# Kernel tuning notes

Hardware: AMD Instinct MI355X
Metric: run time of the kernel (lower is better)

The kernel has to match this reference:

```python
import jax, jax.numpy as jnp
import numpy as np

COMMITMENT_COST = 0.25
NUM_EMBEDDINGS = 8192
EMBEDDING_DIM = 256
N_TOKENS = 32768


def setup_inputs() -> dict:
    key = jax.random.key(0)
    k1, k2 = jax.random.split(key)
    inputs = jax.random.normal(k1, (N_TOKENS, EMBEDDING_DIM), dtype=jnp.float32)
    embed = jax.random.normal(k2, (EMBEDDING_DIM, NUM_EMBEDDINGS), dtype=jnp.float32)
    return {"inputs": inputs, "embed": embed}


def reference(inputs, embed):
    # inputs: [N, D], embed: [D, K]
    input_shape = inputs.shape
    flat = inputs.reshape(-1, embed.shape[0])
    input_norm = jnp.sum(flat * flat, axis=1, keepdims=True)
    embed_norm = jnp.sum(embed * embed, axis=0, keepdims=True)
    distances = input_norm + embed_norm - 2.0 * (flat @ embed)
    encoding_indices = jnp.argmin(distances, axis=1)  # [N]
    # direct gather instead of one-hot matmul (same math)
    quantized = jnp.take(embed.T, encoding_indices, axis=0).reshape(input_shape)
    e_latent_loss = jnp.mean((jax.lax.stop_gradient(quantized) - inputs) ** 2)
    loss = COMMITMENT_COST * e_latent_loss
    # straight-through estimator
    quantized_st = inputs + jax.lax.stop_gradient(quantized - inputs)
    return quantized_st, loss, encoding_indices
```

## Files before the change

### kernel.cpp

```cpp
#include <hip/hip_runtime.h>

#define N_TOK 32768
#define DIM   256
#define NEMB  8192

#define MARGIN_A  0.2f
#define MARGIN_T2 0.008f
#define MARGIN_B  0.0625f
#define GROUP 8
#define KSPLIT 4

typedef _Float16 f16;
typedef __attribute__((ext_vector_type(4))) _Float16 f16x4;
typedef __attribute__((ext_vector_type(8))) _Float16 f16x8;
typedef __attribute__((ext_vector_type(4))) float     f32x4;

__global__ void enorm_kernel(const float* __restrict__ E, float* __restrict__ enorm) {
    int k = blockIdx.x * blockDim.x + threadIdx.x;
    float s = 0.f;
#pragma unroll 8
    for (int d = 0; d < DIM; ++d) {
        float e = E[d * NEMB + k];
        s = fmaf(e, e, s);
    }
    enorm[k] = s;
}

__global__ __launch_bounds__(256) void cvt3_kernel(const float* __restrict__ E,
                                                   f16* __restrict__ ET,
                                                   f16* __restrict__ ETlo,
                                                   float* __restrict__ ET32,
                                                   int wlo, int wf32) {
    __shared__ float shf[64][65];
    const int tid = threadIdx.x;
    const int k0 = (blockIdx.x & 127) * 64;
    const int d0 = (blockIdx.x >> 7) * 64;
#pragma unroll
    for (int i = 0; i < 16; ++i) {
        int flat = i * 256 + tid;
        int k = flat & 63, d = flat >> 6;
        shf[k][d] = E[(size_t)(d0 + d) * NEMB + k0 + k];
    }
    __syncthreads();
#pragma unroll
    for (int i = 0; i < 16; ++i) {
        int flat = i * 256 + tid;
        int d = flat & 63, kk = flat >> 6;
        float v = shf[kk][d];
        f16 hi = (f16)v;
        ET[(size_t)(k0 + kk) * DIM + d0 + d] = hi;
        if (wlo)  ETlo[(size_t)(k0 + kk) * DIM + d0 + d] = (f16)(v - (float)hi);
        if (wf32) ET32[(size_t)(k0 + kk) * DIM + d0 + d] = v;
    }
}

__device__ __forceinline__ void gload_lds16(const void* g, void* l) {
    __builtin_amdgcn_global_load_lds(
        (const __attribute__((address_space(1))) unsigned int*)g,
        (__attribute__((address_space(3))) unsigned int*)l, 16, 0, 0);
}

__global__ __launch_bounds__(512, 2) void argmin_f16v5_kernel(
        const float* __restrict__ X, const f16* __restrict__ ET,
        const float* __restrict__ enorm,
        int* __restrict__ idx1o, int* __restrict__ idx2o, int* __restrict__ flago) {
    __shared__ char smem[131072];

    const int tid = threadIdx.x;
    const int w   = tid >> 6;
    const int l   = tid & 63;
    const int l15 = l & 15, l4 = l >> 4;
    const int h   = w & 1;
    const int cs  = w >> 1;
    const int r0  = blockIdx.x * 128;

    {
        const float4* X4 = (const float4*)(X + (size_t)r0 * DIM);
        f16* xs = (f16*)smem;
#pragma unroll
        for (int i = 0; i < 16; ++i) {
            int flat4 = tid + i * 512;
            float4 v = X4[flat4];
            int row = flat4 >> 6, d4 = flat4 & 63;
            f16x4 p = {(f16)v.x, (f16)v.y, (f16)v.z, (f16)v.w};
            *(f16x4*)(xs + row * 256 + d4 * 4) = p;
        }
    }
    __syncthreads();

    f16x8 Afr[4][8];
    {
        const f16* xs = (const f16*)smem;
#pragma unroll
        for (int mt = 0; mt < 4; ++mt)
#pragma unroll
            for (int c = 0; c < 8; ++c)
                Afr[mt][c] = *(const f16x8*)(xs + (h * 64 + mt * 16 + l15) * 256 + c * 32 + l4 * 8);
    }
    __syncthreads();

    float m1v[4][4], m2v[4][4];
    int   i1v[4][4];
#pragma unroll
    for (int mt = 0; mt < 4; ++mt)
#pragma unroll
        for (int rg = 0; rg < 4; ++rg) {
            m1v[mt][rg] = 3.4e38f; m2v[mt][rg] = 3.4e38f; i1v[mt][rg] = 0x7fffffff;
        }

    auto stagePair = [&](int pt, int buf) {
#pragma unroll
        for (int t = 0; t < 2; ++t) {
            const int kt = pt * 2 + t;
#pragma unroll
            for (int j = 0; j < 4; ++j) {
                const int code = w * 8 + j * 2 + (l >> 5);
                const f16* src = ET + ((size_t)kt * 64 + code) * 256
                                   + (((l & 31) ^ (code & 7)) << 3);
                char* dst = smem + buf * 65536 + t * 32768 + (w * 8 + j * 2) * 512;
                gload_lds16(src, dst);
            }
        }
    };

    const int codeL = cs * 16 + l15;
    stagePair(0, 0);
    int p = 0;
    for (int pt = 0; pt < 64; ++pt) {
        __syncthreads();
        if (pt + 1 < 64) stagePair(pt + 1, p ^ 1);

#pragma unroll
        for (int t = 0; t < 2; ++t) {
            const int kt = pt * 2 + t;
            f32x4 acc[4];
#pragma unroll
            for (int mt = 0; mt < 4; ++mt) acc[mt] = (f32x4){0.f, 0.f, 0.f, 0.f};

            const f16* bb = (const f16*)(smem + p * 65536 + t * 32768);
#pragma unroll
            for (int c = 0; c < 8; ++c) {
                const int g = (c * 4 + l4) ^ (l15 & 7);
                f16x8 b = *(const f16x8*)(bb + codeL * 256 + g * 8);
#pragma unroll
                for (int mt = 0; mt < 4; ++mt)
                    acc[mt] = __builtin_amdgcn_mfma_f32_16x16x32_f16(Afr[mt][c], b, acc[mt], 0, 0, 0);
            }

            const int code = kt * 64 + codeL;
            const float en = enorm[code];
#pragma unroll
            for (int mt = 0; mt < 4; ++mt)
#pragma unroll
                for (int rg = 0; rg < 4; ++rg) {
                    float v = fmaf(-2.f, acc[mt][rg], en);
                    bool cl = v < m1v[mt][rg];
                    m2v[mt][rg] = fminf(m2v[mt][rg], fmaxf(m1v[mt][rg], v));
                    i1v[mt][rg] = cl ? code : i1v[mt][rg];
                    m1v[mt][rg] = fminf(m1v[mt][rg], v);
                }
        }
        p ^= 1;
    }

#pragma unroll
    for (int off = 1; off < 16; off <<= 1) {
#pragma unroll
        for (int mt = 0; mt < 4; ++mt)
#pragma unroll
            for (int rg = 0; rg < 4; ++rg) {
                float om1 = __shfl_xor(m1v[mt][rg], off);
                int   oi1 = __shfl_xor(i1v[mt][rg], off);
                float om2 = __shfl_xor(m2v[mt][rg], off);
                bool sw = (om1 < m1v[mt][rg]) ||
                          (om1 == m1v[mt][rg] && oi1 < i1v[mt][rg]);
                float hi = sw ? m1v[mt][rg] : om1;
                m1v[mt][rg] = sw ? om1 : m1v[mt][rg];
                i1v[mt][rg] = sw ? oi1 : i1v[mt][rg];
                m2v[mt][rg] = fminf(fminf(m2v[mt][rg], om2), hi);
            }
    }

    __syncthreads();
    float* sm1 = (float*)smem;
    int*   si1 = (int*)(smem + 2048);
    float* sm2 = (float*)(smem + 4096);
    if (l15 == 0) {
#pragma unroll
        for (int mt = 0; mt < 4; ++mt)
#pragma unroll
            for (int rg = 0; rg < 4; ++rg) {
                int row = h * 64 + mt * 16 + l4 * 4 + rg;
                sm1[row * 4 + cs] = m1v[mt][rg];
                si1[row * 4 + cs] = i1v[mt][rg];
                sm2[row * 4 + cs] = m2v[mt][rg];
            }
    }
    __syncthreads();
    if (tid < 128) {
        float M1 = 3.4e38f, M2 = 3.4e38f;
        int   I1 = 0x7fffffff;
#pragma unroll
        for (int e = 0; e < 4; ++e) {
            float v = sm1[tid * 4 + e]; int vi = si1[tid * 4 + e];
            if (v < M1 || (v == M1 && vi < I1)) { M2 = M1; M1 = v; I1 = vi; }
            else M2 = fminf(M2, v);
            M2 = fminf(M2, sm2[tid * 4 + e]);
        }
        int r = r0 + tid;
        idx1o[r] = I1;
        idx2o[r] = I1;
        flago[r] = (M2 - M1 < MARGIN_A) ? -1 : 0;
    }
}

__global__ __launch_bounds__(256) void compact_kernel(const int* __restrict__ flago,
        int* __restrict__ list, int* __restrict__ countp) {
    __shared__ int cnts[256], bases[256];
    const int tid = threadIdx.x;
    int c = 0;
    for (int i = 0; i < N_TOK / 256; ++i)
        c += (flago[tid * (N_TOK / 256) + i] < 0) ? 1 : 0;
    cnts[tid] = c;
    __syncthreads();
    if (tid == 0) {
        int run = 0;
        for (int t = 0; t < 256; ++t) { bases[t] = run; run += cnts[t]; }
        countp[0] = run;
    }
    __syncthreads();
    int o = bases[tid];
    for (int i = 0; i < N_TOK / 256; ++i) {
        int r = tid * (N_TOK / 256) + i;
        if (flago[r] < 0) list[o++] = r;
    }
}

__global__ __launch_bounds__(512) void rescan_split_kernel(
        const float* __restrict__ X, const f16* __restrict__ ET,
        const f16* __restrict__ ETlo, const float* __restrict__ enorm,
        const int* __restrict__ list, const int* __restrict__ countp,
        float* __restrict__ pm1, float* __restrict__ pm2, float* __restrict__ pm3,
        int* __restrict__ pi1, int* __restrict__ pi2) {
    __shared__ char smem[131072];
    const int cnt = countp[0];
    const int rb  = blockIdx.x >> 3;
    const int ks  = blockIdx.x & 7;
    if (rb * 64 >= cnt) return;

    const int tid = threadIdx.x, w = tid >> 6, l = tid & 63;
    const int l15 = l & 15, l4 = l >> 4;
    const int h = w & 1, cs = w >> 1;

    f16x8 Ah[2][8], Al[2][8];
#pragma unroll
    for (int mt = 0; mt < 2; ++mt) {
        int jg  = rb * 64 + h * 32 + mt * 16 + l15;
        int row = list[jg < cnt ? jg : cnt - 1];
        const float* xp = X + (size_t)row * DIM + l4 * 8;
#pragma unroll
        for (int c = 0; c < 8; ++c) {
            float4 v0 = *(const float4*)(xp + c * 32);
            float4 v1 = *(const float4*)(xp + c * 32 + 4);
            float xv[8] = {v0.x, v0.y, v0.z, v0.w, v1.x, v1.y, v1.z, v1.w};
            f16x8 hi, lo;
#pragma unroll
            for (int i = 0; i < 8; ++i) {
                f16 hv = (f16)xv[i];
                hi[i] = hv;
                lo[i] = (f16)(xv[i] - (float)hv);
            }
            Ah[mt][c] = hi; Al[mt][c] = lo;
        }
    }

    float m1v[2][4], m2v[2][4], m3v[2][4];
    int   i1v[2][4], i2v[2][4];
#pragma unroll
    for (int mt = 0; mt < 2; ++mt)
#pragma unroll
        for (int rg = 0; rg < 4; ++rg) {
            m1v[mt][rg] = 3.4e38f; m2v[mt][rg] = 3.4e38f; m3v[mt][rg] = 3.4e38f;
            i1v[mt][rg] = 0x7fffffff; i2v[mt][rg] = 0x7fffffff;
        }

    auto stage = [&](int kt, int buf) {
        const int tile = ks * 16 + kt;
#pragma unroll
        for (int j = 0; j < 4; ++j) {
            const int code = w * 8 + j * 2 + (l >> 5);
            size_t off = ((size_t)tile * 64 + code) * 256 + (((l & 31) ^ (code & 7)) << 3);
            char* dsth = smem + buf * 65536 + (w * 8 + j * 2) * 512;
            gload_lds16(ET + off, dsth);
            gload_lds16(ETlo + off, dsth + 32768);
        }
    };

    const int codeL = cs * 16 + l15;
    stage(0, 0);
    int p = 0;
    for (int kt = 0; kt < 16; ++kt) {
        __syncthreads();
        if (kt + 1 < 16) stage(kt + 1, p ^ 1);

        f32x4 acc[2];
#pragma unroll
        for (int mt = 0; mt < 2; ++mt) acc[mt] = (f32x4){0.f, 0.f, 0.f, 0.f};

        const f16* bh = (const f16*)(smem + p * 65536);
        const f16* bl = (const f16*)(smem + p * 65536 + 32768);
#pragma unroll
        for (int c = 0; c < 8; ++c) {
            const int g = (c * 4 + l4) ^ (l15 & 7);
            f16x8 vh = *(const f16x8*)(bh + codeL * 256 + g * 8);
            f16x8 vl = *(const f16x8*)(bl + codeL * 256 + g * 8);
#pragma unroll
            for (int mt = 0; mt < 2; ++mt) {
                acc[mt] = __builtin_amdgcn_mfma_f32_16x16x32_f16(Ah[mt][c], vh, acc[mt], 0, 0, 0);
                acc[mt] = __builtin_amdgcn_mfma_f32_16x16x32_f16(Ah[mt][c], vl, acc[mt], 0, 0, 0);
                acc[mt] = __builtin_amdgcn_mfma_f32_16x16x32_f16(Al[mt][c], vh, acc[mt], 0, 0, 0);
            }
        }

        const int code = (ks * 16 + kt) * 64 + codeL;
        const float en = enorm[code];
#pragma unroll
        for (int mt = 0; mt < 2; ++mt)
#pragma unroll
            for (int rg = 0; rg < 4; ++rg) {
                float v = fmaf(-2.f, acc[mt][rg], en);
                if (v < m1v[mt][rg]) {
                    m3v[mt][rg] = m2v[mt][rg];
                    m2v[mt][rg] = m1v[mt][rg]; i2v[mt][rg] = i1v[mt][rg];
                    m1v[mt][rg] = v;           i1v[mt][rg] = code;
                } else if (v < m2v[mt][rg]) {
                    m3v[mt][rg] = m2v[mt][rg];
                    m2v[mt][rg] = v;           i2v[mt][rg] = code;
                } else if (v < m3v[mt][rg]) {
                    m3v[mt][rg] = v;
                }
            }
        p ^= 1;
    }

    __syncthreads();
    float* Mm1 = (float*)smem;
    int*   Mi1 = (int*)(smem + 16384);
    float* Mm2 = (float*)(smem + 32768);
    int*   Mi2 = (int*)(smem + 49152);
    float* Mm3 = (float*)(smem + 65536);
#pragma unroll
    for (int mt = 0; mt < 2; ++mt)
#pragma unroll
        for (int rg = 0; rg < 4; ++rg) {
            int row = h * 32 + mt * 16 + l4 * 4 + rg;
            int e   = cs * 16 + l15;
            Mm1[row * 64 + e] = m1v[mt][rg];
            Mi1[row * 64 + e] = i1v[mt][rg];
            Mm2[row * 64 + e] = m2v[mt][rg];
            Mi2[row * 64 + e] = i2v[mt][rg];
            Mm3[row * 64 + e] = m3v[mt][rg];
        }
    __syncthreads();
    if (tid < 64) {
        float a1 = 3.4e38f, a2 = 3.4e38f, a3 = 3.4e38f;
        int   ai1 = 0x7fffffff, ai2 = 0x7fffffff;
        for (int e = 0; e < 64; ++e) {
            float b1 = Mm1[tid * 64 + e], b2 = Mm2[tid * 64 + e], b3 = Mm3[tid * 64 + e];
            int   bi1 = Mi1[tid * 64 + e], bi2 = Mi2[tid * 64 + e];
            if (b1 < a1 || (b1 == a1 && bi1 < ai1)) { a3 = a2; a2 = a1; ai2 = ai1; a1 = b1; ai1 = bi1; }
            else if (b1 < a2 || (b1 == a2 && bi1 < ai2)) { a3 = a2; a2 = b1; ai2 = bi1; }
            else if (b1 < a3) a3 = b1;
            if (b2 < a1 || (b2 == a1 && bi2 < ai1)) { a3 = a2; a2 = a1; ai2 = ai1; a1 = b2; ai1 = bi2; }
            else if (b2 < a2 || (b2 == a2 && bi2 < ai2)) { a3 = a2; a2 = b2; ai2 = bi2; }
            else if (b2 < a3) a3 = b2;
            if (b3 < a3) a3 = b3;
        }
        int jg = rb * 64 + tid;
        if (jg < cnt) {
            pm1[jg * 8 + ks] = a1; pm2[jg * 8 + ks] = a2; pm3[jg * 8 + ks] = a3;
            pi1[jg * 8 + ks] = ai1; pi2[jg * 8 + ks] = ai2;
        }
    }
}

__global__ void merge3_kernel(const int* __restrict__ list, const int* __restrict__ countp,
        const float* __restrict__ pm1, const float* __restrict__ pm2,
        const float* __restrict__ pm3,
        const int* __restrict__ pi1, const int* __restrict__ pi2,
        int* __restrict__ idx1o, int* __restrict__ idx2o, int* __restrict__ flago) {
    const int gid = blockIdx.x * 256 + threadIdx.x;
    if (gid >= countp[0]) return;
    float a1 = 3.4e38f, a2 = 3.4e38f, a3 = 3.4e38f;
    int   ai1 = 0x7fffffff, ai2 = 0x7fffffff;
#pragma unroll
    for (int ks = 0; ks < 8; ++ks) {
        float b1 = pm1[gid * 8 + ks], b2 = pm2[gid * 8 + ks], b3 = pm3[gid * 8 + ks];
        int   bi1 = pi1[gid * 8 + ks], bi2 = pi2[gid * 8 + ks];
        if (b1 < a1 || (b1 == a1 && bi1 < ai1)) { a3 = a2; a2 = a1; ai2 = ai1; a1 = b1; ai1 = bi1; }
        else if (b1 < a2 || (b1 == a2 && bi1 < ai2)) { a3 = a2; a2 = b1; ai2 = bi1; }
        else if (b1 < a3) a3 = b1;
        if (b2 < a1 || (b2 == a1 && bi2 < ai1)) { a3 = a2; a2 = a1; ai2 = ai1; a1 = b2; ai1 = bi2; }
        else if (b2 < a2 || (b2 == a2 && bi2 < ai2)) { a3 = a2; a2 = b2; ai2 = bi2; }
        else if (b2 < a3) a3 = b2;
        if (b3 < a3) a3 = b3;
    }
    const int row = list[gid];
    int fl = 0;
    if (a2 - a1 < MARGIN_T2) fl = (a3 - a1 < MARGIN_T2) ? 2 : 1;
    idx1o[row] = ai1; idx2o[row] = ai2; flago[row] = fl;
}

__global__ __launch_bounds__(256) void rescan_group_kernel(
        const float* __restrict__ X, const float* __restrict__ E,
        const float* __restrict__ enorm,
        const int* __restrict__ list, const int* __restrict__ countp,
        float* __restrict__ pm1, float* __restrict__ pm2, float* __restrict__ pm3,
        int* __restrict__ pi1, int* __restrict__ pi2) {
    const int cnt = countp[0];
    const int rc  = blockIdx.x >> 2;
    const int ks  = blockIdx.x & 3;
    if (rc * GROUP >= cnt) return;
    const int tid = threadIdx.x;
    __shared__ int rows_s[GROUP];
    __shared__ float sm1[256], sm2[256], sm3[256];
    __shared__ int   si1[256], si2[256];
    if (tid < GROUP) {
        int j = rc * GROUP + tid;
        rows_s[tid] = list[j < cnt ? j : cnt - 1];
    }
    __syncthreads();
    int rowsg[GROUP];
#pragma unroll
    for (int rr = 0; rr < GROUP; ++rr)
        rowsg[rr] = __builtin_amdgcn_readfirstlane(rows_s[rr]);

    float m1[GROUP], m2[GROUP], m3[GROUP];
    int   i1[GROUP], i2[GROUP];
#pragma unroll
    for (int rr = 0; rr < GROUP; ++rr) {
        m1[rr] = 3.4e38f; m2[rr] = 3.4e38f; m3[rr] = 3.4e38f;
        i1[rr] = 0x7fffffff; i2[rr] = 0x7fffffff;
    }
    for (int j = 0; j < 8; ++j) {
        const int k = ks * 2048 + j * 256 + tid;
        float acc[GROUP];
#pragma unroll
        for (int rr = 0; rr < GROUP; ++rr) acc[rr] = 0.f;
#pragma unroll 1
        for (int dc = 0; dc < 8; ++dc) {
            float ev[32];
#pragma unroll
            for (int i = 0; i < 32; ++i) ev[i] = E[(size_t)(dc * 32 + i) * NEMB + k];
#pragma unroll
            for (int rr = 0; rr < GROUP; ++rr) {
                const float* xp = X + (size_t)rowsg[rr] * DIM + dc * 32;
#pragma unroll
                for (int i = 0; i < 32; ++i) acc[rr] = fmaf(ev[i], xp[i], acc[rr]);
            }
        }
        const float en = enorm[k];
#pragma unroll
        for (int rr = 0; rr < GROUP; ++rr) {
            float v = fmaf(-2.f, acc[rr], en);
            if (v < m1[rr])      { m3[rr] = m2[rr]; m2[rr] = m1[rr]; i2[rr] = i1[rr]; m1[rr] = v; i1[rr] = k; }
            else if (v < m2[rr]) { m3[rr] = m2[rr]; m2[rr] = v; i2[rr] = k; }
            else if (v < m3[rr]) { m3[rr] = v; }
        }
    }
#pragma unroll 1
    for (int rr = 0; rr < GROUP; ++rr) {
        sm1[tid] = m1[rr]; sm2[tid] = m2[rr]; sm3[tid] = m3[rr];
        si1[tid] = i1[rr]; si2[tid] = i2[rr];
        __syncthreads();
        for (int st = 128; st > 0; st >>= 1) {
            if (tid < st) {
                float a1 = sm1[tid], a2 = sm2[tid], a3 = sm3[tid];
                int   ai1 = si1[tid], ai2 = si2[tid];
                float b1 = sm1[tid + st], b2 = sm2[tid + st], b3 = sm3[tid + st];
                int   bi1 = si1[tid + st], bi2 = si2[tid + st];
                if (b1 < a1 || (b1 == a1 && bi1 < ai1)) { a3 = a2; a2 = a1; ai2 = ai1; a1 = b1; ai1 = bi1; }
                else if (b1 < a2 || (b1 == a2 && bi1 < ai2)) { a3 = a2; a2 = b1; ai2 = bi1; }
                else if (b1 < a3) a3 = b1;
                if (b2 < a1 || (b2 == a1 && bi2 < ai1)) { a3 = a2; a2 = a1; ai2 = ai1; a1 = b2; ai1 = bi2; }
                else if (b2 < a2 || (b2 == a2 && bi2 < ai2)) { a3 = a2; a2 = b2; ai2 = bi2; }
                else if (b2 < a3) a3 = b2;
                if (b3 < a3) a3 = b3;
                sm1[tid] = a1; sm2[tid] = a2; sm3[tid] = a3; si1[tid] = ai1; si2[tid] = ai2;
            }
            __syncthreads();
        }
        if (tid == 0) {
            int jg = rc * GROUP + rr;
            if (jg < cnt) {
                pm1[jg * KSPLIT + ks] = sm1[0]; pm2[jg * KSPLIT + ks] = sm2[0];
                pm3[jg * KSPLIT + ks] = sm3[0];
                pi1[jg * KSPLIT + ks] = si1[0]; pi2[jg * KSPLIT + ks] = si2[0];
            }
        }
        __syncthreads();
    }
}

__global__ void merge_kernel(const int* __restrict__ list, const int* __restrict__ countp,
        const float* __restrict__ pm1, const float* __restrict__ pm2,
        const float* __restrict__ pm3,
        const int* __restrict__ pi1, const int* __restrict__ pi2,
        int* __restrict__ idx1o, int* __restrict__ idx2o, int* __restrict__ flago) {
    const int gid = blockIdx.x * 256 + threadIdx.x;
    if (gid >= countp[0]) return;
    float a1 = 3.4e38f, a2 = 3.4e38f, a3 = 3.4e38f;
    int   ai1 = 0x7fffffff, ai2 = 0x7fffffff;
#pragma unroll
    for (int ks = 0; ks < KSPLIT; ++ks) {
        float b1 = pm1[gid * KSPLIT + ks], b2 = pm2[gid * KSPLIT + ks], b3 = pm3[gid * KSPLIT + ks];
        int   bi1 = pi1[gid * KSPLIT + ks], bi2 = pi2[gid * KSPLIT + ks];
        if (b1 < a1 || (b1 == a1 && bi1 < ai1)) { a3 = a2; a2 = a1; ai2 = ai1; a1 = b1; ai1 = bi1; }
        else if (b1 < a2 || (b1 == a2 && bi1 < ai2)) { a3 = a2; a2 = b1; ai2 = bi1; }
        else if (b1 < a3) a3 = b1;
        if (b2 < a1 || (b2 == a1 && bi2 < ai1)) { a3 = a2; a2 = a1; ai2 = ai1; a1 = b2; ai1 = bi2; }
        else if (b2 < a2 || (b2 == a2 && bi2 < ai2)) { a3 = a2; a2 = b2; ai2 = bi2; }
        else if (b2 < a3) a3 = b2;
        if (b3 < a3) a3 = b3;
    }
    const int row = list[gid];
    int fl = 0;
    if (a2 - a1 < MARGIN_B) fl = (a3 - a1 < MARGIN_B) ? 2 : 1;
    idx1o[row] = ai1; idx2o[row] = ai2; flago[row] = fl;
}

#define BM 64
#define BN 128
#define DC 32
#define TM 4
#define TN 8
__global__ __launch_bounds__(256, 2) void argmin_f32_kernel(
        const float* __restrict__ X, const float* __restrict__ E,
        const float* __restrict__ enorm,
        int* __restrict__ idx1o, int* __restrict__ idx2o, int* __restrict__ flago) {
    __shared__ float As[DIM * BM];
    __shared__ float Bs[DC * BN];
    const int tid = threadIdx.x;
    const int r0  = blockIdx.x * BM;
    {
        const float4* X4 = (const float4*)(X + (size_t)r0 * DIM);
#pragma unroll
        for (int i = 0; i < 16; ++i) {
            int flat = tid + i * 256;
            int row = flat >> 6, c4 = flat & 63;
            float4 v = X4[flat];
            int d = c4 * 4;
            As[(d + 0) * BM + row] = v.x;
            As[(d + 1) * BM + row] = v.y;
            As[(d + 2) * BM + row] = v.z;
            As[(d + 3) * BM + row] = v.w;
        }
    }
    const int tc = tid & 15;
    const int tr = tid >> 4;
    float m1[TM], m2[TM], m3[TM];
    int   i1[TM], i2[TM];
#pragma unroll
    for (int j = 0; j < TM; ++j) { m1[j] = m2[j] = m3[j] = 3.4e38f; i1[j] = i2[j] = 0x7fffffff; }
    for (int kt = 0; kt < NEMB; kt += BN) {
        float acc[TM][TN];
#pragma unroll
        for (int j = 0; j < TM; ++j)
#pragma unroll
            for (int i = 0; i < TN; ++i) acc[j][i] = 0.f;
        for (int dc = 0; dc < DIM; dc += DC) {
            __syncthreads();
            const float4* E4 = (const float4*)E;
#pragma unroll
            for (int i = 0; i < 4; ++i) {
                int flat = tid + i * 256;
                int dd = flat >> 5, k4 = flat & 31;
                float4 v = E4[(size_t)(dc + dd) * (NEMB / 4) + (kt >> 2) + k4];
                *(float4*)&Bs[dd * BN + k4 * 4] = v;
            }
            __syncthreads();
#pragma unroll
            for (int dd = 0; dd < DC; ++dd) {
                float4 av = *(const float4*)&As[(dc + dd) * BM + tr * TM];
                float4 b0 = *(const float4*)&Bs[dd * BN + tc * TN];
                float4 b1 = *(const float4*)&Bs[dd * BN + tc * TN + 4];
                float a[TM] = {av.x, av.y, av.z, av.w};
                float b[TN] = {b0.x, b0.y, b0.z, b0.w, b1.x, b1.y, b1.z, b1.w};
#pragma unroll
                for (int j = 0; j < TM; ++j)
#pragma unroll
                    for (int i = 0; i < TN; ++i)
                        acc[j][i] = fmaf(a[j], b[i], acc[j][i]);
            }
        }
        float4 e0 = *(const float4*)&enorm[kt + tc * TN];
        float4 e1 = *(const float4*)&enorm[kt + tc * TN + 4];
        float en[TN] = {e0.x, e0.y, e0.z, e0.w, e1.x, e1.y, e1.z, e1.w};
#pragma unroll
        for (int j = 0; j < TM; ++j) {
#pragma unroll
            for (int i = 0; i < TN; ++i) {
                float v = en[i] - 2.f * acc[j][i];
                int k = kt + tc * TN + i;
                if (v < m1[j]) { m3[j] = m2[j]; m2[j] = m1[j]; i2[j] = i1[j]; m1[j] = v; i1[j] = k; }
                else if (v < m2[j]) { m3[j] = m2[j]; m2[j] = v; i2[j] = k; }
                else if (v < m3[j]) { m3[j] = v; }
            }
        }
    }
    __syncthreads();
    float* Mm1 = As;
    float* Mm2 = As + 1024;
    float* Mm3 = As + 2048;
    int*   Mi1 = (int*)(As + 3072);
    int*   Mi2 = (int*)(As + 4096);
#pragma unroll
    for (int j = 0; j < TM; ++j) {
        int row = tr * TM + j;
        Mm1[row * 16 + tc] = m1[j];
        Mm2[row * 16 + tc] = m2[j];
        Mm3[row * 16 + tc] = m3[j];
        Mi1[row * 16 + tc] = i1[j];
        Mi2[row * 16 + tc] = i2[j];
    }
    __syncthreads();
    if (tid < BM) {
        float M1 = 3.4e38f, M2 = 3.4e38f, M3 = 3.4e38f;
        int I1 = 0x7fffffff, I2 = 0x7fffffff;
        for (int e = 0; e < 16; ++e) {
            float v = Mm1[tid * 16 + e]; int vi = Mi1[tid * 16 + e];
            if (v < M1 || (v == M1 && vi < I1)) { M3 = M2; M2 = M1; I2 = I1; M1 = v; I1 = vi; }
            else if (v < M2 || (v == M2 && vi < I2)) { M3 = M2; M2 = v; I2 = vi; }
            else if (v < M3) { M3 = v; }
            v = Mm2[tid * 16 + e]; vi = Mi2[tid * 16 + e];
            if (v < M1 || (v == M1 && vi < I1)) { M3 = M2; M2 = M1; I2 = I1; M1 = v; I1 = vi; }
            else if (v < M2 || (v == M2 && vi < I2)) { M3 = M2; M2 = v; I2 = vi; }
            else if (v < M3) { M3 = v; }
            v = Mm3[tid * 16 + e];
            if (v < M3) M3 = v;
        }
        int r = r0 + tid;
        int fl = 0;
        if (M2 - M1 < MARGIN_B) fl = (M3 - M1 < MARGIN_B) ? 2 : 1;
        idx1o[r] = I1; idx2o[r] = I2; flago[r] = fl;
    }
}

__global__ __launch_bounds__(256) void refine_kernel(
        const float* __restrict__ X, const float* __restrict__ E,
        int* __restrict__ idx1o, const int* __restrict__ idx2o,
        const int* __restrict__ flago) {
    __shared__ double redA[256];
    __shared__ double redB[256];
    __shared__ int    redI[256];
    const int tid = threadIdx.x;
    for (int rr = 0; rr < 8; ++rr) {
        int r = blockIdx.x * 8 + rr;
        int flag = flago[r];
        if (flag == 0) continue;
        if (flag == 1) {
            int a = idx1o[r], b = idx2o[r];
            double x  = (double)X[(size_t)r * DIM + tid];
            double ea = (double)E[(size_t)tid * NEMB + a];
            double eb = (double)E[(size_t)tid * NEMB + b];
            redA[tid] = ea * (ea - 2.0 * x);
            redB[tid] = eb * (eb - 2.0 * x);
            __syncthreads();
            for (int s = 128; s > 0; s >>= 1) {
                if (tid < s) { redA[tid] += redA[tid + s]; redB[tid] += redB[tid + s]; }
                __syncthreads();
            }
            if (tid == 0) {
                double sa = redA[0], sb = redB[0];
                idx1o[r] = (sb < sa || (sb == sa && b < a)) ? b : a;
            }
            __syncthreads();
        } else {
            double bm = 1e300; int bi = 0x7fffffff;
            for (int k = tid; k < NEMB; k += 256) {
                double s = 0.0;
                for (int d = 0; d < DIM; ++d) {
                    double e = (double)E[(size_t)d * NEMB + k];
                    double x = (double)X[(size_t)r * DIM + d];
                    s += e * (e - 2.0 * x);
                }
                if (s < bm) { bm = s; bi = k; }
            }
            redA[tid] = bm; redI[tid] = bi;
            __syncthreads();
            for (int s = 128; s > 0; s >>= 1) {
                if (tid < s) {
                    if (redA[tid + s] < redA[tid] ||
                        (redA[tid + s] == redA[tid] && redI[tid + s] < redI[tid])) {
                        redA[tid] = redA[tid + s]; redI[tid] = redI[tid + s];
                    }
                }
                __syncthreads();
            }
            if (tid == 0) idx1o[r] = redI[0];
            __syncthreads();
        }
    }
}

__global__ __launch_bounds__(256) void gather_kernel(
        const float* __restrict__ X, const float* __restrict__ E,
        const int* __restrict__ idx,
        float* __restrict__ outq, float* __restrict__ outidxf,
        double* __restrict__ partials) {
    __shared__ double red[256];
    const int tid = threadIdx.x;
    const int row = blockIdx.x * 4 + (tid >> 6);
    const int d0  = (tid & 63) * 4;
    const int k   = idx[row];
    float4 x = *(const float4*)&X[(size_t)row * DIM + d0];
    float q0 = E[(size_t)(d0 + 0) * NEMB + k];
    float q1 = E[(size_t)(d0 + 1) * NEMB + k];
    float q2 = E[(size_t)(d0 + 2) * NEMB + k];
    float q3 = E[(size_t)(d0 + 3) * NEMB + k];
    float4 q = {q0, q1, q2, q3};
    *(float4*)&outq[(size_t)row * DIM + d0] = q;
    if ((tid & 63) == 0) outidxf[row] = (float)k;
    double s = 0.0, t;
    t = (double)q0 - (double)x.x; s += t * t;
    t = (double)q1 - (double)x.y; s += t * t;
    t = (double)q2 - (double)x.z; s += t * t;
    t = (double)q3 - (double)x.w; s += t * t;
    red[tid] = s;
    __syncthreads();
    for (int st = 128; st > 0; st >>= 1) {
        if (tid < st) red[tid] += red[tid + st];
        __syncthreads();
    }
    if (tid == 0) partials[blockIdx.x] = red[0];
}

__global__ __launch_bounds__(256) void gather2_kernel(
        const float* __restrict__ X, const float* __restrict__ ET32,
        const int* __restrict__ idx,
        float* __restrict__ outq, float* __restrict__ outidxf,
        double* __restrict__ partials) {
    __shared__ double red[256];
    const int tid = threadIdx.x;
    const int row = blockIdx.x * 4 + (tid >> 6);
    const int d0  = (tid & 63) * 4;
    const int k   = idx[row];
    float4 x = *(const float4*)&X[(size_t)row * DIM + d0];
    float4 q = *(const float4*)&ET32[(size_t)k * DIM + d0];
    *(float4*)&outq[(size_t)row * DIM + d0] = q;
    if ((tid & 63) == 0) outidxf[row] = (float)k;
    double s = 0.0, t;
    t = (double)q.x - (double)x.x; s += t * t;
    t = (double)q.y - (double)x.y; s += t * t;
    t = (double)q.z - (double)x.z; s += t * t;
    t = (double)q.w - (double)x.w; s += t * t;
    red[tid] = s;
    __syncthreads();
    for (int st = 128; st > 0; st >>= 1) {
        if (tid < st) red[tid] += red[tid + st];
        __syncthreads();
    }
    if (tid == 0) partials[blockIdx.x] = red[0];
}

__global__ __launch_bounds__(256) void loss_kernel(const double* __restrict__ partials,
                                                   float* __restrict__ outloss) {
    __shared__ double red[256];
    const int tid = threadIdx.x;
    double s = 0.0;
    for (int i = tid; i < N_TOK / 4; i += 256) s += partials[i];
    red[tid] = s;
    __syncthreads();
    for (int st = 128; st > 0; st >>= 1) {
        if (tid < st) red[tid] += red[tid + st];
        __syncthreads();
    }
    if (tid == 0)
        outloss[0] = (float)(0.25 * red[0] / (double)((size_t)N_TOK * DIM));
}

extern "C" void kernel_launch(void* const* d_in, const int* in_sizes, int n_in,
                              void* d_out, int out_size, void* d_ws, size_t ws_size,
                              hipStream_t stream) {
    const float* X = (const float*)d_in[0];
    const float* E = (const float*)d_in[1];

    float* outq    = (float*)d_out;
    float* outloss = outq + (size_t)N_TOK * DIM;
    float* outidx  = outloss + 1;

    char* base = (char*)d_ws;
    float*  enorm    = (float*)base;
    int*    idx1     = (int*)(base + 32768);
    int*    idx2     = (int*)(base + 163840);
    int*    flag     = (int*)(base + 294912);
    double* partials = (double*)(base + 425984);
    f16*    ET       = (f16*)(base + 524288);
    char*   etbase   = base + 524288;
    int*    listB    = (int*)etbase;
    int*    countB   = (int*)(etbase + 131072);
    float*  pm1B     = (float*)(etbase + 132096);
    float*  pm2B     = (float*)(etbase + 132096 + 524288);
    float*  pm3B     = (float*)(etbase + 132096 + 1048576);
    int*    pi1B     = (int*)  (etbase + 132096 + 1572864);
    int*    pi2B     = (int*)  (etbase + 132096 + 2097152);
    f16*    ETlo     = (f16*)(base + 4718592);
    int*    listA    = (int*)(base + 8912896);
    int*    countA   = (int*)(base + 9043968);
    float*  ET32     = (float*)(base + 9044992);
    float*  pm1A     = outq;
    float*  pm2A     = outq + 262144;
    float*  pm3A     = outq + 524288;
    int*    pi1A     = (int*)(outq + 786432);
    int*    pi2A     = (int*)(outq + 1048576);
    const size_t NEED_B  = 4718592;
    const size_t NEED_A  = 12190720;
    const size_t NEED_A2 = 9044992 + (size_t)NEMB * DIM * sizeof(float);

    enorm_kernel<<<NEMB / 256, 256, 0, stream>>>(E, enorm);
    if (ws_size >= NEED_A) {
        const int wf32 = (ws_size >= NEED_A2) ? 1 : 0;
        cvt3_kernel        <<<512,        256, 0, stream>>>(E, ET, ETlo, ET32, 1, wf32);
        argmin_f16v5_kernel<<<N_TOK / 128, 512, 0, stream>>>(X, ET, enorm, idx1, idx2, flag);
        compact_kernel     <<<1,          256, 0, stream>>>(flag, listA, countA);
        rescan_split_kernel<<<512 * 8,    512, 0, stream>>>(X, ET, ETlo, enorm, listA, countA,
                                                            pm1A, pm2A, pm3A, pi1A, pi2A);
        merge3_kernel      <<<N_TOK / 256, 256, 0, stream>>>(listA, countA, pm1A, pm2A, pm3A,
                                                             pi1A, pi2A, idx1, idx2, flag);
        refine_kernel<<<N_TOK / 8, 256, 0, stream>>>(X, E, idx1, idx2, flag);
        if (wf32)
            gather2_kernel<<<N_TOK / 4, 256, 0, stream>>>(X, ET32, idx1, outq, outidx, partials);
        else
            gather_kernel <<<N_TOK / 4, 256, 0, stream>>>(X, E, idx1, outq, outidx, partials);
    } else if (ws_size >= NEED_B) {
        cvt3_kernel        <<<512,        256, 0, stream>>>(E, ET, ET, (float*)ET, 0, 0);
        argmin_f16v5_kernel<<<N_TOK / 128, 512, 0, stream>>>(X, ET, enorm, idx1, idx2, flag);
        compact_kernel     <<<1,          256, 0, stream>>>(flag, listB, countB);
        rescan_group_kernel<<<(N_TOK / GROUP) * KSPLIT, 256, 0, stream>>>(X, E, enorm, listB, countB,
                                                                          pm1B, pm2B, pm3B, pi1B, pi2B);
        merge_kernel       <<<N_TOK / 256, 256, 0, stream>>>(listB, countB, pm1B, pm2B, pm3B,
                                                             pi1B, pi2B, idx1, idx2, flag);
        refine_kernel<<<N_TOK / 8, 256, 0, stream>>>(X, E, idx1, idx2, flag);
        gather_kernel<<<N_TOK / 4, 256, 0, stream>>>(X, E, idx1, outq, outidx, partials);
    } else {
        argmin_f32_kernel  <<<N_TOK / BM, 256, 0, stream>>>(X, E, enorm, idx1, idx2, flag);
        refine_kernel<<<N_TOK / 8, 256, 0, stream>>>(X, E, idx1, idx2, flag);
        gather_kernel<<<N_TOK / 4, 256, 0, stream>>>(X, E, idx1, outq, outidx, partials);
    }
    loss_kernel  <<<1,         256, 0, stream>>>(partials, outloss);
}
```

Before: 292.3 us.

## Split codebook across two wave halves in 1024-thread argmin blocks

The argmin kernel now launches 1024 threads per block. Each set of 8 waves scans its own half of the codebook (4096 codes) through its own double-buffered 32KB LDS stage, instead of 8 waves walking all codes in pairs of tiles. The final cross-wave reduction grows from 4 to 8 candidates per row. The goal is to double the waves resident per CU under the same 128KB LDS footprint, so more MFMA and load latency can be hidden. The cost is more register pressure from the A fragments duplicated in both halves, and heavier barriers across 16 waves.

```diff
diff --git a/kernel.cpp b/kernel.cpp
--- a/kernel.cpp
+++ b/kernel.cpp
@@ -60,26 +60,28 @@
         (__attribute__((address_space(3))) unsigned int*)l, 16, 0, 0);
 }
 
-__global__ __launch_bounds__(512, 2) void argmin_f16v5_kernel(
+__global__ __launch_bounds__(1024, 4) void argmin_f16v6_kernel(
         const float* __restrict__ X, const f16* __restrict__ ET,
         const float* __restrict__ enorm,
         int* __restrict__ idx1o, int* __restrict__ idx2o, int* __restrict__ flago) {
     __shared__ char smem[131072];
 
-    const int tid = threadIdx.x;
-    const int w   = tid >> 6;
-    const int l   = tid & 63;
-    const int l15 = l & 15, l4 = l >> 4;
-    const int h   = w & 1;
-    const int cs  = w >> 1;
-    const int r0  = blockIdx.x * 128;
+    const int tid  = threadIdx.x;
+    const int w    = tid >> 6;
+    const int l    = tid & 63;
+    const int l15  = l & 15, l4 = l >> 4;
+    const int half = w >> 3;
+    const int w8   = w & 7;
+    const int h    = w8 & 1;
+    const int cs   = w8 >> 1;
+    const int r0   = blockIdx.x * 128;
 
     {
         const float4* X4 = (const float4*)(X + (size_t)r0 * DIM);
         f16* xs = (f16*)smem;
 #pragma unroll
-        for (int i = 0; i < 16; ++i) {
-            int flat4 = tid + i * 512;
+        for (int i = 0; i < 8; ++i) {
+            int flat4 = tid + i * 1024;
             float4 v = X4[flat4];
             int row = flat4 >> 6, d4 = flat4 & 63;
             f16x4 p = {(f16)v.x, (f16)v.y, (f16)v.z, (f16)v.w};
@@ -108,58 +110,50 @@
             m1v[mt][rg] = 3.4e38f; m2v[mt][rg] = 3.4e38f; i1v[mt][rg] = 0x7fffffff;
         }
 
-    auto stagePair = [&](int pt, int buf) {
-#pragma unroll
-        for (int t = 0; t < 2; ++t) {
-            const int kt = pt * 2 + t;
-#pragma unroll
-            for (int j = 0; j < 4; ++j) {
-                const int code = w * 8 + j * 2 + (l >> 5);
-                const f16* src = ET + ((size_t)kt * 64 + code) * 256
-                                   + (((l & 31) ^ (code & 7)) << 3);
-                char* dst = smem + buf * 65536 + t * 32768 + (w * 8 + j * 2) * 512;
-                gload_lds16(src, dst);
-            }
+    auto stage = [&](int kt, int buf) {
+#pragma unroll
+        for (int j = 0; j < 4; ++j) {
+            const int code = w8 * 8 + j * 2 + (l >> 5);
+            const f16* src = ET + ((size_t)(half * 4096 + kt * 64 + code)) * 256
+                               + (((l & 31) ^ (code & 7)) << 3);
+            char* dst = smem + half * 65536 + buf * 32768 + (w8 * 8 + j * 2) * 512;
+            gload_lds16(src, dst);
         }
     };
 
     const int codeL = cs * 16 + l15;
-    stagePair(0, 0);
+    stage(0, 0);
     int p = 0;
-    for (int pt = 0; pt < 64; ++pt) {
+    for (int kt = 0; kt < 64; ++kt) {
         __syncthreads();
-        if (pt + 1 < 64) stagePair(pt + 1, p ^ 1);
-
-#pragma unroll
-        for (int t = 0; t < 2; ++t) {
-            const int kt = pt * 2 + t;
-            f32x4 acc[4];
-#pragma unroll
-            for (int mt = 0; mt < 4; ++mt) acc[mt] = (f32x4){0.f, 0.f, 0.f, 0.f};
-
-            const f16* bb = (const f16*)(smem + p * 65536 + t * 32768);
-#pragma unroll
-            for (int c = 0; c < 8; ++c) {
-                const int g = (c * 4 + l4) ^ (l15 & 7);
-                f16x8 b = *(const f16x8*)(bb + codeL * 256 + g * 8);
-#pragma unroll
-                for (int mt = 0; mt < 4; ++mt)
-                    acc[mt] = __builtin_amdgcn_mfma_f32_16x16x32_f16(Afr[mt][c], b, acc[mt], 0, 0, 0);
-            }
-
-            const int code = kt * 64 + codeL;
-            const float en = enorm[code];
+        if (kt + 1 < 64) stage(kt + 1, p ^ 1);
+
+        f32x4 acc[4];
+#pragma unroll
+        for (int mt = 0; mt < 4; ++mt) acc[mt] = (f32x4){0.f, 0.f, 0.f, 0.f};
+
+        const f16* bb = (const f16*)(smem + half * 65536 + p * 32768);
+#pragma unroll
+        for (int c = 0; c < 8; ++c) {
+            const int g = (c * 4 + l4) ^ (l15 & 7);
+            f16x8 b = *(const f16x8*)(bb + codeL * 256 + g * 8);
 #pragma unroll
             for (int mt = 0; mt < 4; ++mt)
-#pragma unroll
-                for (int rg = 0; rg < 4; ++rg) {
-                    float v = fmaf(-2.f, acc[mt][rg], en);
-                    bool cl = v < m1v[mt][rg];
-                    m2v[mt][rg] = fminf(m2v[mt][rg], fmaxf(m1v[mt][rg], v));
-                    i1v[mt][rg] = cl ? code : i1v[mt][rg];
-                    m1v[mt][rg] = fminf(m1v[mt][rg], v);
-                }
-        }
+                acc[mt] = __builtin_amdgcn_mfma_f32_16x16x32_f16(Afr[mt][c], b, acc[mt], 0, 0, 0);
+        }
+
+        const int code = half * 4096 + kt * 64 + codeL;
+        const float en = enorm[code];
+#pragma unroll
+        for (int mt = 0; mt < 4; ++mt)
+#pragma unroll
+            for (int rg = 0; rg < 4; ++rg) {
+                float v = fmaf(-2.f, acc[mt][rg], en);
+                bool cl = v < m1v[mt][rg];
+                m2v[mt][rg] = fminf(m2v[mt][rg], fmaxf(m1v[mt][rg], v));
+                i1v[mt][rg] = cl ? code : i1v[mt][rg];
+                m1v[mt][rg] = fminf(m1v[mt][rg], v);
+            }
         p ^= 1;
     }
 
@@ -183,17 +177,18 @@
 
     __syncthreads();
     float* sm1 = (float*)smem;
-    int*   si1 = (int*)(smem + 2048);
-    float* sm2 = (float*)(smem + 4096);
+    int*   si1 = (int*)(smem + 4096);
+    float* sm2 = (float*)(smem + 8192);
     if (l15 == 0) {
 #pragma unroll
         for (int mt = 0; mt < 4; ++mt)
 #pragma unroll
             for (int rg = 0; rg < 4; ++rg) {
                 int row = h * 64 + mt * 16 + l4 * 4 + rg;
-                sm1[row * 4 + cs] = m1v[mt][rg];
-                si1[row * 4 + cs] = i1v[mt][rg];
-                sm2[row * 4 + cs] = m2v[mt][rg];
+                int e   = half * 4 + cs;
+                sm1[row * 8 + e] = m1v[mt][rg];
+                si1[row * 8 + e] = i1v[mt][rg];
+                sm2[row * 8 + e] = m2v[mt][rg];
             }
     }
     __syncthreads();
@@ -201,11 +196,11 @@
         float M1 = 3.4e38f, M2 = 3.4e38f;
         int   I1 = 0x7fffffff;
 #pragma unroll
-        for (int e = 0; e < 4; ++e) {
-            float v = sm1[tid * 4 + e]; int vi = si1[tid * 4 + e];
+        for (int e = 0; e < 8; ++e) {
+            float v = sm1[tid * 8 + e]; int vi = si1[tid * 8 + e];
             if (v < M1 || (v == M1 && vi < I1)) { M2 = M1; M1 = v; I1 = vi; }
             else M2 = fminf(M2, v);
-            M2 = fminf(M2, sm2[tid * 4 + e]);
+            M2 = fminf(M2, sm2[tid * 8 + e]);
         }
         int r = r0 + tid;
         idx1o[r] = I1;
@@ -821,7 +816,7 @@
     if (ws_size >= NEED_A) {
         const int wf32 = (ws_size >= NEED_A2) ? 1 : 0;
         cvt3_kernel        <<<512,        256, 0, stream>>>(E, ET, ETlo, ET32, 1, wf32);
-        argmin_f16v5_kernel<<<N_TOK / 128, 512, 0, stream>>>(X, ET, enorm, idx1, idx2, flag);
+        argmin_f16v6_kernel<<<N_TOK / 128, 1024, 0, stream>>>(X, ET, enorm, idx1, idx2, flag);
         compact_kernel     <<<1,          256, 0, stream>>>(flag, listA, countA);
         rescan_split_kernel<<<512 * 8,    512, 0, stream>>>(X, ET, ETlo, enorm, listA, countA,
                                                             pm1A, pm2A, pm3A, pi1A, pi2A);
@@ -834,7 +829,7 @@
             gather_kernel <<<N_TOK / 4, 256, 0, stream>>>(X, E, idx1, outq, outidx, partials);
     } else if (ws_size >= NEED_B) {
         cvt3_kernel        <<<512,        256, 0, stream>>>(E, ET, ET, (float*)ET, 0, 0);
-        argmin_f16v5_kernel<<<N_TOK / 128, 512, 0, stream>>>(X, ET, enorm, idx1, idx2, flag);
+        argmin_f16v6_kernel<<<N_TOK / 128, 1024, 0, stream>>>(X, ET, enorm, idx1, idx2, flag);
         compact_kernel     <<<1,          256, 0, stream>>>(flag, listB, countB);
         rescan_group_kernel<<<(N_TOK / GROUP) * KSPLIT, 256, 0, stream>>>(X, E, enorm, listB, countB,
                                                                           pm1B, pm2B, pm3B, pi1B, pi2B);
```

Result: slower. 1.064 ms (+264.2%).
